# Kernel optimization log

Measured on AMD Instinct MI355X. Metric: run time of the kernel, lower is better.

## Reference

```python
import jax, jax.numpy as jnp
import numpy as np
import math

C = 256

def conv_bn_lrelu(x, w, scale, bias, dilation):
    # Conv2d(k=3, stride=1, padding=dilation, dilation=dilation, bias=False) + eval BN (folded) + LeakyReLU(0.1)
    d = dilation
    y = jax.lax.conv_general_dilated(
        x, w, window_strides=(1, 1), padding=[(d, d), (d, d)],
        rhs_dilation=(d, d), dimension_numbers=('NCHW', 'OIHW', 'NCHW'))
    y = y * scale[None, :, None, None] + bias[None, :, None, None]
    return jnp.where(y > 0, y, 0.1 * y)

def unfold3x3(x):
    # [b,c,h,w] -> [b,c,9,h,w]: 3x3 neighborhoods (zero pad 1), row-major window order like F.unfold
    b, c, h, w = x.shape
    xp = jnp.pad(x, ((0, 0), (0, 0), (1, 1), (1, 1)))
    return jnp.stack([xp[:, :, i:i + h, j:j + w] for i in range(3) for j in range(3)], axis=2)

def self_attn(Q, K, V):
    b, c, h, w = Q.shape
    Ku = unfold3x3(K)                     # [b,c,9,h,w]
    Vu = unfold3x3(V)                     # [b,c,9,h,w]
    dot = Q[:, :, None] * Ku * (1.0 / math.sqrt(c))
    dot = jax.nn.softmax(dot, axis=2)     # softmax over 9 neighbors, per channel
    return jnp.sum(dot * Vu, axis=2)      # [b,c,h,w]

def setup_inputs() -> dict:
    key = jax.random.key(0)
    ks = jax.random.split(key, 20)
    fan = C * 9
    wstd = math.sqrt(2.0 / fan)
    def w(k):
        return jax.random.normal(k, (C, C, 3, 3), dtype=jnp.float32) * wstd
    def s(k):
        return jax.random.uniform(k, (C,), dtype=jnp.float32, minval=0.5, maxval=1.5)
    def b(k):
        return jax.random.normal(k, (C,), dtype=jnp.float32) * 0.1
    inp = {'x': jax.random.normal(ks[0], (4, C, 64, 64), dtype=jnp.float32)}
    names = ['q1', 'k1', 'v1', 'q2', 'k2', 'v2']
    for i, n in enumerate(names):
        inp[n[0] + 'w' + n[1]] = w(ks[1 + 3 * i])
        inp[n[0] + 's' + n[1]] = s(ks[2 + 3 * i])
        inp[n[0] + 'b' + n[1]] = b(ks[3 + 3 * i])
    return inp

def reference(x, qw1, qs1, qb1, kw1, ks1, kb1, vw1, vs1, vb1,
              qw2, qs2, qb2, kw2, ks2, kb2, vw2, vs2, vb2):
    Q1 = conv_bn_lrelu(x, qw1, qs1, qb1, dilation=1)
    K1 = conv_bn_lrelu(x, kw1, ks1, kb1, dilation=1)
    V1 = conv_bn_lrelu(x, vw1, vs1, vb1, dilation=1)
    attn1 = self_attn(Q1, K1, V1)
    Q2 = conv_bn_lrelu(attn1, qw2, qs2, qb2, dilation=2)
    K2 = conv_bn_lrelu(attn1, kw2, ks2, kb2, dilation=2)
    V2 = conv_bn_lrelu(attn1, vw2, vs2, vb2, dilation=2)
    return self_attn(Q2, K2, V2)
```

## Files before the change

### kernel.cpp

```cpp
#include <hip/hip_runtime.h>
#include <stdint.h>

typedef __attribute__((ext_vector_type(8))) short short8;
typedef __attribute__((ext_vector_type(4))) float f32x4;
typedef __attribute__((ext_vector_type(4))) unsigned short u16x4;
typedef __attribute__((ext_vector_type(8))) unsigned short u16x8;

#define DEV static __device__ __forceinline__

DEV unsigned short f2bf(float f) {
  unsigned u = __float_as_uint(f);
  u += 0x7FFFu + ((u >> 16) & 1u);
  return (unsigned short)(u >> 16);
}
DEV float bf2f(unsigned short s) { return __uint_as_float(((unsigned)s) << 16); }

DEV void gload16(const void* g, void* l) {
  __attribute__((address_space(1))) unsigned* gp =
      reinterpret_cast<__attribute__((address_space(1))) unsigned*>(
          reinterpret_cast<uintptr_t>(g));
  __attribute__((address_space(3))) unsigned* lp =
      reinterpret_cast<__attribute__((address_space(3))) unsigned*>(
          reinterpret_cast<uintptr_t>(l));
  __builtin_amdgcn_global_load_lds(gp, lp, 16, 0, 0);
}

__global__ __launch_bounds__(256) void prologue(
    const float* __restrict__ x,
    const float* __restrict__ w0, const float* __restrict__ s0,
    const float* __restrict__ w1, const float* __restrict__ s1,
    const float* __restrict__ w2, const float* __restrict__ s2,
    const float* __restrict__ w3, const float* __restrict__ s3,
    const float* __restrict__ w4, const float* __restrict__ s4,
    const float* __restrict__ w5, const float* __restrict__ s5,
    unsigned short* __restrict__ XP, unsigned short* __restrict__ QP,
    unsigned short* __restrict__ KP, unsigned short* __restrict__ VP,
    unsigned short* __restrict__ AP, unsigned short* __restrict__ W2base) {
  __shared__ float sm[64][65];
  const int blk = blockIdx.x;
  const int t = threadIdx.x;

  if (blk < 1320) {
    const int bx = blk % 66, by = blk / 66;
    const int buf = by >> 2, b = by & 3;
    const int P = (buf == 4) ? 68 : 66;
    const int pad = (buf == 4) ? 2 : 1;
    const int nb = P * P - 64 * 64;
    const int i = bx * 256 + t;
    const int pxi = i >> 5, ch = (i & 31) * 8;
    if (pxi >= nb) return;
    const int topbot = 2 * pad * P;
    int h, w;
    if (pxi < topbot) {
      const int r = pxi / P, c = pxi - r * P;
      h = (r < pad) ? r : P - 2 * pad + r;
      w = c;
    } else {
      const int j = pxi - topbot;
      const int r = j / (2 * pad), c = j - r * 2 * pad;
      h = pad + r;
      w = (c < pad) ? c : P - 2 * pad + c;
    }
    unsigned short* base = buf == 0 ? XP : buf == 1 ? QP : buf == 2 ? KP
                           : buf == 3 ? VP : AP;
    const u16x8 z = {0, 0, 0, 0, 0, 0, 0, 0};
    *(u16x8*)&base[((size_t)(b * P + h) * P + w) * 256 + ch] = z;
  } else if (blk < 2856) {
    const int idx = blk - 1320;
    const int set = idx >> 8, cout = idx & 255;
    const float* wl[6] = {w0, w1, w2, w3, w4, w5};
    const float* sl[6] = {s0, s1, s2, s3, s4, s5};
    const float sc = sl[set][cout];
    const float* src = wl[set] + ((size_t)cout * 256 + t) * 9;
    float v[9];
#pragma unroll
    for (int k = 0; k < 9; ++k) v[k] = src[k] * sc;
    unsigned short* dst =
        W2base + (size_t)set * 256 * 2304 + (size_t)cout * 2304;
#pragma unroll
    for (int k = 0; k < 9; ++k) dst[k * 256 + t] = f2bf(v[k]);
  } else {
    const int bid = blk - 2856;
    const int ct = bid & 3;
    const int h = (bid >> 2) & 63;
    const int b = bid >> 8;
    const int wl2 = t & 63, cr = t >> 6;
#pragma unroll
    for (int cc = 0; cc < 16; ++cc) {
      const int c = cc * 4 + cr;
      sm[c][wl2] = x[((size_t)(b * 256 + ct * 64 + c) * 64 + h) * 64 + wl2];
    }
    __syncthreads();
    const int ww = t >> 2, c16 = (t & 3) * 16;
    u16x8 o0, o1;
#pragma unroll
    for (int i = 0; i < 8; ++i) o0[i] = f2bf(sm[c16 + i][ww]);
#pragma unroll
    for (int i = 0; i < 8; ++i) o1[i] = f2bf(sm[c16 + 8 + i][ww]);
    const size_t base =
        ((size_t)(b * 66 + h + 1) * 66 + (ww + 1)) * 256 + ct * 64 + c16;
    *(u16x8*)&XP[base] = o0;
    *(u16x8*)&XP[base + 8] = o1;
  }
}

template <int D>
__global__ __launch_bounds__(256, 2) void conv_qkv(
    const unsigned short* __restrict__ Xp, const unsigned short* __restrict__ Wq,
    const unsigned short* __restrict__ Wk, const unsigned short* __restrict__ Wv,
    const float* __restrict__ bq, const float* __restrict__ bk,
    const float* __restrict__ bv, unsigned short* __restrict__ Qo,
    unsigned short* __restrict__ Ko, unsigned short* __restrict__ Vo) {
  constexpr int P = 64 + 2 * D;
  constexpr int HALF = 128 * 64 + 3 * 64 * 64;
  __shared__ __align__(16) unsigned short lds[2 * HALF];

  const int tid = threadIdx.x;
  const int lane = tid & 63;
  const int wid = tid >> 6;
  const int wm = wid >> 1;
  const int wn = wid & 1;
  const int wgid = blockIdx.x;
  const int xcd = wgid & 7;
  const int m0 = (xcd & 3) * 64;
  const int rg = (wgid >> 3) + 64 * (xcd >> 2);
  const int b = rg >> 5;
  const int h0 = (rg & 31) * 2;

  f32x4 acc[3][2][4];
#pragma unroll
  for (int c = 0; c < 3; ++c)
#pragma unroll
    for (int m = 0; m < 2; ++m)
#pragma unroll
      for (int n = 0; n < 4; ++n) acc[c][m][n] = (f32x4){0.f, 0.f, 0.f, 0.f};

  const int w0i = tid >> 3;
  const int j3 = (tid & 7) ^ (w0i & 7);
  const unsigned short* wptr[3] = {Wq, Wk, Wv};
  size_t bRow[2];
#pragma unroll
  for (int r = 0; r < 2; ++r)
    bRow[r] = ((size_t)(b * P + h0 + r) * P + w0i) * 256 + j3 * 8;
  const size_t aBase = (size_t)(m0 + w0i) * 2304 + j3 * 8;

  auto STAGE = [&](int s, int hf) {
    const int t = s >> 2, kb = s & 3;
    const int ty = t / 3, tx = t - ty * 3;
    const size_t tapOff = ((size_t)(ty * D) * P + tx * D) * 256 + kb * 64;
    const int kOff = t * 256 + kb * 64;
    unsigned short* base = &lds[hf * HALF];
#pragma unroll
    for (int k = 0; k < 4; ++k)
      gload16(Xp + bRow[k >> 1] + (size_t)(32 * (k & 1)) * 256 + tapOff,
              &base[(k * 256 + tid) * 8]);
#pragma unroll
    for (int k = 0; k < 6; ++k)
      gload16(wptr[k >> 1] + aBase + (size_t)(k & 1) * 32 * 2304 + kOff,
              &base[8192 + (k * 256 + tid) * 8]);
  };

  auto COMPUTE = [&](int hf) {
    const unsigned short* base = &lds[hf * HALF];
#pragma unroll
    for (int kk = 0; kk < 2; ++kk) {
      const int jc = kk * 4 + (lane >> 4);
      short8 bfr[4], afr[3][2];
#pragma unroll
      for (int n = 0; n < 4; ++n) {
        const int row = wn * 64 + n * 16 + (lane & 15);
        bfr[n] = *(const short8*)&base[row * 64 + ((jc ^ (row & 7)) << 3)];
      }
#pragma unroll
      for (int c = 0; c < 3; ++c)
#pragma unroll
        for (int m = 0; m < 2; ++m) {
          const int row = wm * 32 + m * 16 + (lane & 15);
          afr[c][m] = *(const short8*)&base[8192 + c * 4096 + row * 64 +
                                            ((jc ^ (row & 7)) << 3)];
        }
      __builtin_amdgcn_s_setprio(1);
#pragma unroll
      for (int c = 0; c < 3; ++c)
#pragma unroll
        for (int m = 0; m < 2; ++m)
#pragma unroll
          for (int n = 0; n < 4; ++n)
            acc[c][m][n] = __builtin_amdgcn_mfma_f32_16x16x32_bf16(
                afr[c][m], bfr[n], acc[c][m][n], 0, 0, 0);
      __builtin_amdgcn_s_setprio(0);
    }
  };

  STAGE(0, 0);
#pragma unroll 1
  for (int s = 0; s < 35; ++s) {
    const int p = s & 1;
    STAGE(s + 1, p ^ 1);
    asm volatile("s_waitcnt vmcnt(10)" ::: "memory");
    __builtin_amdgcn_s_barrier();
    COMPUTE(p);
    __builtin_amdgcn_s_barrier();
  }
  asm volatile("s_waitcnt vmcnt(0)" ::: "memory");
  __builtin_amdgcn_s_barrier();
  COMPUTE(1);

  const float* bias[3] = {bq, bk, bv};
  unsigned short* outp[3] = {Qo, Ko, Vo};
  const int r4 = (lane >> 4) << 2;
#pragma unroll
  for (int c = 0; c < 3; ++c) {
#pragma unroll
    for (int m = 0; m < 2; ++m) {
      const int cout = m0 + wm * 32 + m * 16 + r4;
      const f32x4 bb = *(const f32x4*)&bias[c][cout];
#pragma unroll
      for (int n = 0; n < 4; ++n) {
        const int px = wn * 64 + n * 16 + (lane & 15);
        const int ww = px & 63;
        const int hh = h0 + (px >> 6);
        const size_t off =
            ((size_t)(b * 66 + hh + 1) * 66 + (ww + 1)) * 256 + cout;
        u16x4 pk;
#pragma unroll
        for (int r = 0; r < 4; ++r) {
          float f = acc[c][m][n][r] + bb[r];
          f = f > 0.f ? f : 0.1f * f;
          pk[r] = f2bf(f);
        }
        *(u16x4*)&outp[c][off] = pk;
      }
    }
  }
}

template <int MODE>
__global__ __launch_bounds__(256) void attn3x3(
    const unsigned short* __restrict__ Qp, const unsigned short* __restrict__ Kp,
    const unsigned short* __restrict__ Vp, unsigned short* __restrict__ outB,
    float* __restrict__ outF) {
  __shared__ float so[8][257];
  const int tid = threadIdx.x;
  const int bid = ((blockIdx.x & 7) << 8) + (blockIdx.x >> 3);
  const int gid = bid * 256 + tid;
  const int cch = gid & 31;
  const int pix = gid >> 5;
  const int b = pix >> 12, h = (pix >> 6) & 63, w = pix & 63;
  const int c0 = cch * 8;

  const size_t cen = ((size_t)(b * 66 + h + 1) * 66 + (w + 1)) * 256 + c0;
  const size_t tl = ((size_t)(b * 66 + h) * 66 + w) * 256 + c0;

  float q[8];
  {
    u16x8 u = *(const u16x8*)&Qp[cen];
#pragma unroll
    for (int i = 0; i < 8; ++i) q[i] = bf2f(u[i]) * 0.0625f;
  }
  float s[9][8];
#pragma unroll
  for (int t = 0; t < 9; ++t) {
    u16x8 u = *(const u16x8*)&Kp[tl + (size_t)((t / 3) * 66 + (t % 3)) * 256];
#pragma unroll
    for (int i = 0; i < 8; ++i) s[t][i] = q[i] * bf2f(u[i]);
  }
  float mx[8];
#pragma unroll
  for (int i = 0; i < 8; ++i) {
    float m = s[0][i];
#pragma unroll
    for (int t = 1; t < 9; ++t) m = fmaxf(m, s[t][i]);
    mx[i] = m;
  }
  float num[8], den[8];
#pragma unroll
  for (int i = 0; i < 8; ++i) { num[i] = 0.f; den[i] = 0.f; }
#pragma unroll
  for (int t = 0; t < 9; ++t) {
    u16x8 u = *(const u16x8*)&Vp[tl + (size_t)((t / 3) * 66 + (t % 3)) * 256];
#pragma unroll
    for (int i = 0; i < 8; ++i) {
      const float e = __expf(s[t][i] - mx[i]);
      den[i] += e;
      num[i] += e * bf2f(u[i]);
    }
  }

  if (MODE == 0) {
    u16x8 o;
#pragma unroll
    for (int i = 0; i < 8; ++i)
      o[i] = f2bf(num[i] * __builtin_amdgcn_rcpf(den[i]));
    *(u16x8*)&outB[((size_t)(b * 68 + h + 2) * 68 + (w + 2)) * 256 + c0] = o;
  } else {
    const int ps = tid >> 5;
#pragma unroll
    for (int i = 0; i < 8; ++i)
      so[ps][c0 + i] = num[i] * __builtin_amdgcn_rcpf(den[i]);
    __syncthreads();
    const int pix0 = bid * 8;
    const int b2 = pix0 >> 12, h2 = (pix0 >> 6) & 63, w0 = pix0 & 63;
    const int c = tid;
    const size_t ob = (((size_t)b2 * 256 + c) * 64 + h2) * 64 + w0;
    f32x4 v0 = (f32x4){so[0][c], so[1][c], so[2][c], so[3][c]};
    f32x4 v1 = (f32x4){so[4][c], so[5][c], so[6][c], so[7][c]};
    *(f32x4*)&outF[ob] = v0;
    *(f32x4*)&outF[ob + 4] = v1;
  }
}

extern "C" void kernel_launch(void* const* d_in, const int* in_sizes, int n_in,
                              void* d_out, int out_size, void* d_ws,
                              size_t ws_size, hipStream_t stream) {
  (void)in_sizes; (void)n_in; (void)out_size; (void)ws_size;
  const float* x = (const float*)d_in[0];
  const float* wqs[6] = {(const float*)d_in[1],  (const float*)d_in[4],
                         (const float*)d_in[7],  (const float*)d_in[10],
                         (const float*)d_in[13], (const float*)d_in[16]};
  const float* scs[6] = {(const float*)d_in[2],  (const float*)d_in[5],
                         (const float*)d_in[8],  (const float*)d_in[11],
                         (const float*)d_in[14], (const float*)d_in[17]};
  const float* bq1 = (const float*)d_in[3];
  const float* bk1 = (const float*)d_in[6];
  const float* bv1 = (const float*)d_in[9];
  const float* bq2 = (const float*)d_in[12];
  const float* bk2 = (const float*)d_in[15];
  const float* bv2 = (const float*)d_in[18];

  char* ws = (char*)d_ws;
  const size_t SZ66 = (size_t)4 * 66 * 66 * 256 * 2;
  const size_t SZ68 = (size_t)4 * 68 * 68 * 256 * 2;
  unsigned short* XP = (unsigned short*)(ws);
  unsigned short* QP = (unsigned short*)(ws + SZ66);
  unsigned short* KP = (unsigned short*)(ws + 2 * SZ66);
  unsigned short* VP = (unsigned short*)(ws + 3 * SZ66);
  unsigned short* AP = (unsigned short*)(ws + 4 * SZ66);
  const size_t wbase = 4 * SZ66 + SZ68;
  unsigned short* W2base = (unsigned short*)(ws + wbase);
  const size_t WSET = (size_t)256 * 2304;

  prologue<<<3880, 256, 0, stream>>>(
      x, wqs[0], scs[0], wqs[1], scs[1], wqs[2], scs[2], wqs[3], scs[3],
      wqs[4], scs[4], wqs[5], scs[5], XP, QP, KP, VP, AP, W2base);

  conv_qkv<1><<<512, 256, 0, stream>>>(
      XP, W2base, W2base + WSET, W2base + 2 * WSET, bq1, bk1, bv1, QP, KP, VP);
  attn3x3<0><<<2048, 256, 0, stream>>>(QP, KP, VP, AP, nullptr);
  conv_qkv<2><<<512, 256, 0, stream>>>(
      AP, W2base + 3 * WSET, W2base + 4 * WSET, W2base + 5 * WSET, bq2, bk2,
      bv2, QP, KP, VP);
  attn3x3<1><<<2048, 256, 0, stream>>>(QP, KP, VP, nullptr, (float*)d_out);
}
```

Baseline: 152.4 us.

## Load conv weight fragments directly from global into registers, skipping LDS staging

The Q/K/V weight tiles are no longer staged through shared memory with global_load_lds. Each wave now reads its MFMA A-fragments straight from global memory into double-buffered registers one step ahead. LDS holds only the activation tile, which shrinks shared memory per block and removes the LDS reads for the weights. In exchange it adds 24 short8 registers per thread plus uncoalesced-ish per-lane global reads of weights that are duplicated across waves, and the vmcnt wait count has been retuned.

```diff
diff --git a/kernel.cpp b/kernel.cpp
--- a/kernel.cpp
+++ b/kernel.cpp
@@ -112,7 +112,7 @@
     const float* __restrict__ bv, unsigned short* __restrict__ Qo,
     unsigned short* __restrict__ Ko, unsigned short* __restrict__ Vo) {
   constexpr int P = 64 + 2 * D;
-  constexpr int HALF = 128 * 64 + 3 * 64 * 64;
+  constexpr int HALF = 128 * 64;
   __shared__ __align__(16) unsigned short lds[2 * HALF];
 
   const int tid = threadIdx.x;
@@ -142,43 +142,47 @@
 #pragma unroll
   for (int r = 0; r < 2; ++r)
     bRow[r] = ((size_t)(b * P + h0 + r) * P + w0i) * 256 + j3 * 8;
-  const size_t aBase = (size_t)(m0 + w0i) * 2304 + j3 * 8;
-
-  auto STAGE = [&](int s, int hf) {
+  size_t aRow[2];
+#pragma unroll
+  for (int m = 0; m < 2; ++m)
+    aRow[m] = (size_t)(m0 + wm * 32 + m * 16 + (lane & 15)) * 2304 +
+              (lane >> 4) * 8;
+
+  auto STAGE_B = [&](int s, int hf) {
     const int t = s >> 2, kb = s & 3;
     const int ty = t / 3, tx = t - ty * 3;
     const size_t tapOff = ((size_t)(ty * D) * P + tx * D) * 256 + kb * 64;
-    const int kOff = t * 256 + kb * 64;
     unsigned short* base = &lds[hf * HALF];
 #pragma unroll
     for (int k = 0; k < 4; ++k)
       gload16(Xp + bRow[k >> 1] + (size_t)(32 * (k & 1)) * 256 + tapOff,
               &base[(k * 256 + tid) * 8]);
-#pragma unroll
-    for (int k = 0; k < 6; ++k)
-      gload16(wptr[k >> 1] + aBase + (size_t)(k & 1) * 32 * 2304 + kOff,
-              &base[8192 + (k * 256 + tid) * 8]);
   };
 
-  auto COMPUTE = [&](int hf) {
+  auto LOAD_A = [&](int s, short8 (&a)[12]) {
+    const int t = s >> 2, kb = s & 3;
+    const int kOff = t * 256 + kb * 64;
+#pragma unroll
+    for (int c = 0; c < 3; ++c)
+#pragma unroll
+      for (int m = 0; m < 2; ++m)
+#pragma unroll
+        for (int kk = 0; kk < 2; ++kk)
+          a[c * 4 + m * 2 + kk] =
+              *(const short8*)&wptr[c][aRow[m] + kOff + kk * 32];
+  };
+
+  auto COMPUTE = [&](int hf, const short8 (&a)[12]) {
     const unsigned short* base = &lds[hf * HALF];
 #pragma unroll
     for (int kk = 0; kk < 2; ++kk) {
       const int jc = kk * 4 + (lane >> 4);
-      short8 bfr[4], afr[3][2];
+      short8 bfr[4];
 #pragma unroll
       for (int n = 0; n < 4; ++n) {
         const int row = wn * 64 + n * 16 + (lane & 15);
         bfr[n] = *(const short8*)&base[row * 64 + ((jc ^ (row & 7)) << 3)];
       }
-#pragma unroll
-      for (int c = 0; c < 3; ++c)
-#pragma unroll
-        for (int m = 0; m < 2; ++m) {
-          const int row = wm * 32 + m * 16 + (lane & 15);
-          afr[c][m] = *(const short8*)&base[8192 + c * 4096 + row * 64 +
-                                            ((jc ^ (row & 7)) << 3)];
-        }
       __builtin_amdgcn_s_setprio(1);
 #pragma unroll
       for (int c = 0; c < 3; ++c)
@@ -187,24 +191,35 @@
 #pragma unroll
           for (int n = 0; n < 4; ++n)
             acc[c][m][n] = __builtin_amdgcn_mfma_f32_16x16x32_bf16(
-                afr[c][m], bfr[n], acc[c][m][n], 0, 0, 0);
+                a[c * 4 + m * 2 + kk], bfr[n], acc[c][m][n], 0, 0, 0);
       __builtin_amdgcn_s_setprio(0);
     }
   };
 
-  STAGE(0, 0);
+  short8 aP[12], aQ[12];
+
+  auto STEP = [&](int s, const short8 (&aCur)[12], short8 (&aNxt)[12]) {
+    const int hf = s & 1;
+    if (s < 35) {
+      STAGE_B(s + 1, hf ^ 1);
+      LOAD_A(s + 1, aNxt);
+      asm volatile("s_waitcnt vmcnt(16)" ::: "memory");
+    } else {
+      asm volatile("s_waitcnt vmcnt(0)" ::: "memory");
+    }
+    __builtin_amdgcn_sched_barrier(0);
+    __builtin_amdgcn_s_barrier();
+    COMPUTE(hf, aCur);
+    __builtin_amdgcn_s_barrier();
+  };
+
+  STAGE_B(0, 0);
+  LOAD_A(0, aP);
 #pragma unroll 1
-  for (int s = 0; s < 35; ++s) {
-    const int p = s & 1;
-    STAGE(s + 1, p ^ 1);
-    asm volatile("s_waitcnt vmcnt(10)" ::: "memory");
-    __builtin_amdgcn_s_barrier();
-    COMPUTE(p);
-    __builtin_amdgcn_s_barrier();
-  }
-  asm volatile("s_waitcnt vmcnt(0)" ::: "memory");
-  __builtin_amdgcn_s_barrier();
-  COMPUTE(1);
+  for (int su = 0; su < 18; ++su) {
+    STEP(su * 2, aP, aQ);
+    STEP(su * 2 + 1, aQ, aP);
+  }
 
   const float* bias[3] = {bq, bk, bv};
   unsigned short* outp[3] = {Qo, Ko, Vo};
```

New measurement: 413.9 us. 172% more time.
